# Optimization experiments

Hardware: AMD Instinct MI355X
Metric: run time of the kernel (lower is better)

The kernel has to match this reference:

```python
import jax, jax.numpy as jnp
import numpy as np

# Config: B sequences, each of length S; paged KV cache with NB blocks of size BS.
B, S, HQ, HK, D = 4, 1024, 32, 8, 128
BS = 256
NB = B * (S // BS)  # 16 blocks, one contiguous run per sequence
SCALE = 1.0 / float(np.sqrt(D))


def setup_inputs() -> dict:
    key = jax.random.key(0)
    k1, k2, k3 = jax.random.split(key, 3)
    q = jax.random.normal(k1, (B * S, HQ, D), dtype=jnp.float32)
    k_cache = jax.random.normal(k2, (NB, BS, HK, D), dtype=jnp.float32)
    v_cache = jax.random.normal(k3, (NB, BS, HK, D), dtype=jnp.float32)
    # block_table[b, j] = physical block id of j-th logical block of sequence b
    block_table = jnp.arange(B * (S // BS), dtype=jnp.int32).reshape(B, S // BS)
    return {"q": q, "k_cache": k_cache, "v_cache": v_cache, "block_table": block_table}


def reference(q, k_cache, v_cache, block_table):
    # Equivalent of pytorch_attn_varlen_func (prefill, causal, paged KV, GQA)
    # with equal per-sequence lengths, vectorized over the batch dim.
    Bn, nblk = block_table.shape
    _, BSc, Hk, Dd = k_cache.shape
    Sl = nblk * BSc
    Hq = q.shape[1]
    g = Hq // Hk  # GQA group size

    qb = q.reshape(Bn, Sl, Hq, Dd)  # [B, S, Hq, D]

    # Paged gather: token t -> block block_table[b, t // BS], offset t % BS
    t = jnp.arange(Sl)
    bids = block_table[:, t // BSc]          # [B, S]
    off = t % BSc                             # [S]
    kb = k_cache[bids, off[None, :]]          # [B, S, Hk, D]
    vb = v_cache[bids, off[None, :]]

    # Align KV heads to query heads (repeat_interleave over head dim)
    kb = jnp.repeat(kb, g, axis=2)            # [B, S, Hq, D]
    vb = jnp.repeat(vb, g, axis=2)

    scores = jnp.einsum('bqhd,bkhd->bhqk', qb, kb).astype(jnp.float32) * SCALE
    causal_mask = jnp.arange(Sl)[None, :] > jnp.arange(Sl)[:, None]  # [Sq, Sk]
    scores = jnp.where(causal_mask[None, None], -jnp.inf, scores)
    attn = jax.nn.softmax(scores, axis=-1).astype(q.dtype)  # [B, Hq, S, S]
    out = jnp.einsum('bhqk,bkhd->bqhd', attn, vb)            # [B, S, Hq, D]
    return out.reshape(Bn * Sl, Hq * Dd)
```

## Files before the change

kernel.cpp:

```cpp
#include <hip/hip_runtime.h>


#define SEQ   1024
#define NHQ   32
#define NHK   8
#define DH    128
#define BSZ   256
#define NBLK  16
#define QBLK  128
#define KVBLK 64
#define SCALE  0.0883883476483184f
#define SCLOG2 0.12752551286084812f

typedef __attribute__((ext_vector_type(8)))  short bf16x8;
typedef __attribute__((ext_vector_type(4)))  float f32x4;
typedef __attribute__((ext_vector_type(16))) float f32x16;
typedef __attribute__((ext_vector_type(2)))  unsigned int u32x2;
typedef unsigned short u16;
typedef unsigned int u32;
typedef unsigned long long u64;

static __device__ __forceinline__ u16 f2bf(float f) {
  union { float f; u32 u; } x; x.f = f;
  return (u16)((x.u + 0x7fffu + ((x.u >> 16) & 1u)) >> 16);
}

static __device__ __forceinline__ u32 cvtpk(float a, float b) {
  u32 r;
  asm("v_cvt_pk_bf16_f32 %0, %1, %2" : "=v"(r) : "v"(a), "v"(b));
  return r;
}

static __device__ __forceinline__ void gload16(const u16* src, u16* dst_lds) {
  __builtin_amdgcn_global_load_lds(
      (const __attribute__((address_space(1))) u32*)src,
      (__attribute__((address_space(3))) u32*)dst_lds, 16, 0, 0);
}

__global__ __launch_bounds__(256)
void prep_kv(const float* __restrict__ kc_, const float* __restrict__ vc_,
             u16* __restrict__ kb, u16* __restrict__ vbT) {
  __shared__ u16 lvt[64 * 132];

  const int t  = threadIdx.x;
  const int blk = blockIdx.x;
  const int t4 = blk & 3;
  const int hk = (blk >> 2) & 7;
  const int nb = blk >> 5;
  const int key0 = t4 * 64;

  const int d4 = t & 31;
  const int kr = t >> 5;

#pragma unroll
  for (int i = 0; i < 8; ++i) {
    const int key = kr + i * 8;
    const size_t srow = ((size_t)(nb * BSZ + key0 + key) * NHK + hk) * DH + 4 * d4;
    f32x4 kx = *(const f32x4*)(kc_ + srow);
    f32x4 vx = *(const f32x4*)(vc_ + srow);
    u64 pk = (u64)f2bf(kx[0]) | ((u64)f2bf(kx[1]) << 16) |
             ((u64)f2bf(kx[2]) << 32) | ((u64)f2bf(kx[3]) << 48);
    *(u64*)(kb + (((size_t)(nb * NHK + hk) * BSZ + key0 + key) * DH + 4 * d4)) = pk;
    u64 pv = (u64)f2bf(vx[0]) | ((u64)f2bf(vx[1]) << 16) |
             ((u64)f2bf(vx[2]) << 32) | ((u64)f2bf(vx[3]) << 48);
    *(u64*)&lvt[key * 132 + 4 * d4] = pv;
  }
  __syncthreads();

  const int d  = t >> 1;
  const int h2 = t & 1;
  u16* dst = vbT + ((size_t)(nb * NHK + hk) * DH + d) * BSZ + key0 + h2 * 32;
  u64 outw[8];
#pragma unroll
  for (int j = 0; j < 8; ++j) {
    const int kbase = h2 * 32 + j * 4;
    outw[j] = (u64)lvt[(kbase + 0) * 132 + d]
            | ((u64)lvt[(kbase + 1) * 132 + d] << 16)
            | ((u64)lvt[(kbase + 2) * 132 + d] << 32)
            | ((u64)lvt[(kbase + 3) * 132 + d] << 48);
  }
#pragma unroll
  for (int j = 0; j < 8; ++j) ((u64*)dst)[j] = outw[j];
}

__global__ __launch_bounds__(256, 2)
void attn_fwd_pre(const float* __restrict__ qg,
                  const u16* __restrict__ kbg,
                  const u16* __restrict__ vbT,
                  const int* __restrict__ btab,
                  float* __restrict__ outg)
{
  __shared__ u16 lk[2][KVBLK * DH];
  __shared__ u16 lv[2][DH * KVBLK];

  const int tid  = threadIdx.x;
  const int lane = tid & 63;
  const int w    = tid >> 6;
  const int ln   = lane & 31;
  const int hi   = lane >> 5;
  const int bid  = blockIdx.x;

  const int qc = 7 - (bid >> 7);
  const int rr = bid & 127;
  const int hq = rr >> 2;
  const int b  = rr & 3;
  const int hk = hq >> 2;

  const int rg = qc * QBLK + w * 32 + ln;

  bf16x8 qf[8];
  {
    const float* qp = qg + ((size_t)(b * SEQ + rg) * NHQ + hq) * DH;
#pragma unroll
    for (int dc = 0; dc < 8; ++dc) {
      const int d0 = dc * 16 + hi * 8;
      f32x4 x0 = *(const f32x4*)(qp + d0);
      f32x4 x1 = *(const f32x4*)(qp + d0 + 4);
      bf16x8 f;
#pragma unroll
      for (int j = 0; j < 4; ++j) {
        f[j]     = (short)f2bf(x0[j] * SCLOG2);
        f[j + 4] = (short)f2bf(x1[j] * SCLOG2);
      }
      qf[dc] = f;
    }
  }

  bf16x8 onesf;
#pragma unroll
  for (int j = 0; j < 8; ++j) onesf[j] = (short)0x3F80;

  f32x16 o[4];
#pragma unroll
  for (int db = 0; db < 4; ++db)
#pragma unroll
    for (int i = 0; i < 16; ++i) o[db][i] = 0.f;
  f32x16 lacc;
#pragma unroll
  for (int i = 0; i < 16; ++i) lacc[i] = 0.f;

  const u16* kbh = kbg + (size_t)hk * BSZ * DH;
  const u16* vbh = vbT + (size_t)hk * DH * BSZ;

  auto stage_k = [&](int t, int c) {
    const int nb   = btab[b * (SEQ / BSZ) + (t >> 2)];
    const int off0 = (t & 3) * KVBLK;
    const u16* ksrc = kbh + (size_t)nb * (NHK * BSZ * DH) + (size_t)off0 * DH;
#pragma unroll
    for (int i = 0; i < 4; ++i) {
      const int kbs = w * 16 + i * 4;
      const int key = kbs + (lane >> 4);
      const u16* src = ksrc + key * DH + 8 * ((lane & 15) ^ (key & 15));
      gload16(src, &lk[c][kbs * DH]);
    }
  };
  auto stage_v = [&](int t, int c) {
    const int nb   = btab[b * (SEQ / BSZ) + (t >> 2)];
    const int off0 = (t & 3) * KVBLK;
    const u16* vsrc = vbh + (size_t)nb * (NHK * DH * BSZ) + off0;
#pragma unroll
    for (int i = 0; i < 4; ++i) {
      const int dbs = w * 32 + i * 8;
      const int d   = dbs + (lane >> 3);
      const u16* src = vsrc + d * BSZ + 8 * ((lane & 7) ^ (d & 7));
      gload16(src, &lv[c][dbs * KVBLK]);
    }
  };

  const int ntile = 2 * qc + 2;
  const int tmaxw = 2 * qc + (w >> 1);

  auto qk = [&](int tt, int cc, f32x16& s0, f32x16& s1) {
    if (tt <= tmaxw) {
      __builtin_amdgcn_s_setprio(1);
#pragma unroll
      for (int kb = 0; kb < 2; ++kb) {
        f32x16 acc;
#pragma unroll
        for (int i = 0; i < 16; ++i) acc[i] = 0.f;
        const int key  = kb * 32 + ln;
        const int srow = key * DH;
        const int sw   = (key & 15) * 8;
#pragma unroll
        for (int dc = 0; dc < 8; ++dc) {
          const int d0 = dc * 16 + hi * 8;
          bf16x8 kf = *(const bf16x8*)&lk[cc][srow + (d0 ^ sw)];
          acc = __builtin_amdgcn_mfma_f32_32x32x16_bf16(kf, qf[dc], acc, 0, 0, 0);
        }
        if (kb == 0) s0 = acc; else s1 = acc;
      }
      __builtin_amdgcn_s_setprio(0);
      if (tt == tmaxw) {
        const int kt = tt * KVBLK;
#pragma unroll
        for (int r = 0; r < 16; ++r) {
          const int kg0 = kt + (r & 3) + 8 * (r >> 2) + 4 * hi;
          if (kg0 > rg)      s0[r] = -1e30f;
          if (kg0 + 32 > rg) s1[r] = -1e30f;
        }
      }
    } else {
#pragma unroll
      for (int i = 0; i < 16; ++i) { s0[i] = -1e30f; s1[i] = -1e30f; }
    }
  };

  auto pv = [&](f32x16& p0, f32x16& p1, int cc) {
#pragma unroll
    for (int kc = 0; kc < 4; ++kc) {
      const int cc2 = kc & 1;
      const f32x16& sa0 = (kc < 2) ? p0 : p1;
      const u32 x0 = cvtpk(sa0[8 * cc2 + 0], sa0[8 * cc2 + 1]);
      const u32 y0 = cvtpk(sa0[8 * cc2 + 4], sa0[8 * cc2 + 5]);
      const u32 x1 = cvtpk(sa0[8 * cc2 + 2], sa0[8 * cc2 + 3]);
      const u32 y1 = cvtpk(sa0[8 * cc2 + 6], sa0[8 * cc2 + 7]);
      u32x2 r0 = __builtin_amdgcn_permlane32_swap(x0, y0, false, false);
      u32x2 r1 = __builtin_amdgcn_permlane32_swap(x1, y1, false, false);
      union { bf16x8 v; u32 u[4]; } pb;
      pb.u[0] = r0[0]; pb.u[1] = r1[0]; pb.u[2] = r0[1]; pb.u[3] = r1[1];
      const int k0 = kc * 16 + hi * 8;
      __builtin_amdgcn_s_setprio(1);
#pragma unroll
      for (int db = 0; db < 4; ++db) {
        const int d = db * 32 + ln;
        bf16x8 vf = *(const bf16x8*)&lv[cc][d * KVBLK + (k0 ^ ((d & 7) * 8))];
        o[db] = __builtin_amdgcn_mfma_f32_32x32x16_bf16(vf, pb.v, o[db], 0, 0, 0);
      }
      lacc = __builtin_amdgcn_mfma_f32_32x32x16_bf16(onesf, pb.v, lacc, 0, 0, 0);
      __builtin_amdgcn_s_setprio(0);
    }
  };

  stage_k(0, 0);
  if (1 < ntile) stage_k(1, 1);
  stage_v(0, 0);
  if (1 < ntile) stage_v(1, 1);
  __syncthreads();

  for (int t = 0; t < ntile; t += 2) {
    const bool liveA = (t <= tmaxw);
    const bool liveB = (t + 1 <= tmaxw);

    f32x16 sA0, sA1, sB0, sB1;
    qk(t,     0, sA0, sA1);
    qk(t + 1, 1, sB0, sB1);

    __syncthreads();

    if (t + 2 < ntile) stage_k(t + 2, 0);
    if (t + 3 < ntile) stage_k(t + 3, 1);

    if (liveA) {
#pragma unroll
      for (int i = 0; i < 16; ++i) {
        sA0[i] = exp2f(sA0[i]);
        sA1[i] = exp2f(sA1[i]);
      }
      if (liveB) {
#pragma unroll
        for (int i = 0; i < 16; ++i) {
          sB0[i] = exp2f(sB0[i]);
          sB1[i] = exp2f(sB1[i]);
        }
      }

      pv(sA0, sA1, 0);
      if (liveB) pv(sB0, sB1, 1);
    }

    __syncthreads();

    if (t + 2 < ntile) stage_v(t + 2, 0);
    if (t + 3 < ntile) stage_v(t + 3, 1);
  }

  const float inv = 1.0f / lacc[0];
  float* op = outg + ((size_t)(b * SEQ + rg) * NHQ + hq) * DH;
#pragma unroll
  for (int db = 0; db < 4; ++db)
#pragma unroll
    for (int q4 = 0; q4 < 4; ++q4) {
      f32x4 val;
#pragma unroll
      for (int r2 = 0; r2 < 4; ++r2) val[r2] = o[db][q4 * 4 + r2] * inv;
      *(f32x4*)(op + db * 32 + q4 * 8 + hi * 4) = val;
    }
}

__global__ __launch_bounds__(256, 2)
void attn_fwd_fb(const float* __restrict__ qg,
                 const float* __restrict__ kcache,
                 const float* __restrict__ vcache,
                 const int*   __restrict__ btab,
                 float* __restrict__ outg)
{
  __shared__ u16 lk[KVBLK * DH];
  __shared__ u16 lv[DH * KVBLK];
  __shared__ u16 lp[4][16 * KVBLK];

  const int tid  = threadIdx.x;
  const int lane = tid & 63;
  const int w    = tid >> 6;
  const int qt   = blockIdx.x;
  const int hq   = blockIdx.y;
  const int b    = blockIdx.z;
  const int hk   = hq >> 2;
  const int qbase = qt * 64;
  const int cl = lane & 15;
  const int kg = lane >> 4;

  bf16x8 qf[4];
  {
    const int tq = qbase + w * 16 + cl;
    const float* qp = qg + ((size_t)(b * SEQ + tq) * NHQ + hq) * DH;
#pragma unroll
    for (int dc = 0; dc < 4; ++dc) {
      const int d0 = dc * 32 + kg * 8;
      f32x4 x0 = *(const f32x4*)(qp + d0);
      f32x4 x1 = *(const f32x4*)(qp + d0 + 4);
      bf16x8 f;
#pragma unroll
      for (int j = 0; j < 4; ++j) { f[j] = (short)f2bf(x0[j] * SCALE); f[j + 4] = (short)f2bf(x1[j] * SCALE); }
      qf[dc] = f;
    }
  }

  f32x4 o[8];
#pragma unroll
  for (int i = 0; i < 8; ++i) o[i] = (f32x4){0.f, 0.f, 0.f, 0.f};
  float mrow[4] = {-1e30f, -1e30f, -1e30f, -1e30f};
  float lrow[4] = {0.f, 0.f, 0.f, 0.f};

  const int ntile = qt + 1;
  for (int t = 0; t < ntile; ++t) {
    __syncthreads();
    {
      const int nb   = btab[b * (SEQ / BSZ) + ((t * KVBLK) / BSZ)];
      const int off0 = (t * KVBLK) % BSZ;
      const int d4 = tid & 31;
      const int kl = tid >> 5;
      const float* kbp = kcache + (((size_t)nb * BSZ + off0) * NHK + hk) * DH + d4 * 4;
      const float* vbp = vcache + (((size_t)nb * BSZ + off0) * NHK + hk) * DH + d4 * 4;
#pragma unroll
      for (int p = 0; p < 8; ++p) {
        const int key = p * 8 + kl;
        const size_t go = (size_t)key * (NHK * DH);
        f32x4 kx = *(const f32x4*)(kbp + go);
        f32x4 vx = *(const f32x4*)(vbp + go);
        u32 w0 = (u32)f2bf(kx[0]) | ((u32)f2bf(kx[1]) << 16);
        u32 w1 = (u32)f2bf(kx[2]) | ((u32)f2bf(kx[3]) << 16);
        const int doff = (4 * d4) ^ ((key & 7) * 8);
        u64 pk = (u64)w0 | ((u64)w1 << 32);
        *(u64*)&lk[key * DH + doff] = pk;
#pragma unroll
        for (int j = 0; j < 4; ++j) {
          const int d = 4 * d4 + j;
          lv[d * KVBLK + (key ^ ((d & 7) * 8))] = f2bf(vx[j]);
        }
      }
    }
    __syncthreads();

    float s[4][4];
#pragma unroll
    for (int ct = 0; ct < 4; ++ct) {
      f32x4 acc = (f32x4){0.f, 0.f, 0.f, 0.f};
      const int key = ct * 16 + cl;
#pragma unroll
      for (int dc = 0; dc < 4; ++dc) {
        const int d0 = (dc * 32 + kg * 8) ^ ((key & 7) * 8);
        bf16x8 kf = *(const bf16x8*)&lk[key * DH + d0];
        acc = __builtin_amdgcn_mfma_f32_16x16x32_bf16(qf[dc], kf, acc, 0, 0, 0);
      }
#pragma unroll
      for (int v = 0; v < 4; ++v) s[ct][v] = acc[v];
    }
    if (t == qt) {
      const int rbase = w * 16 + kg * 4;
#pragma unroll
      for (int ct = 0; ct < 4; ++ct) {
        const int key = ct * 16 + cl;
#pragma unroll
        for (int v = 0; v < 4; ++v)
          if (key > rbase + v) s[ct][v] = -1e30f;
      }
    }
    float corr[4];
#pragma unroll
    for (int v = 0; v < 4; ++v) {
      float x = fmaxf(fmaxf(s[0][v], s[1][v]), fmaxf(s[2][v], s[3][v]));
#pragma unroll
      for (int off = 1; off < 16; off <<= 1) x = fmaxf(x, __shfl_xor(x, off));
      const float mn = fmaxf(mrow[v], x);
      corr[v] = __expf(mrow[v] - mn);
      mrow[v] = mn;
    }
    float rs[4] = {0.f, 0.f, 0.f, 0.f};
    u16 pb[4][4];
#pragma unroll
    for (int ct = 0; ct < 4; ++ct)
#pragma unroll
      for (int v = 0; v < 4; ++v) {
        const float p = __expf(s[ct][v] - mrow[v]);
        rs[v] += p;
        pb[ct][v] = f2bf(p);
      }
#pragma unroll
    for (int v = 0; v < 4; ++v) {
      float x = rs[v];
#pragma unroll
      for (int off = 1; off < 16; off <<= 1) x += __shfl_xor(x, off);
      lrow[v] = lrow[v] * corr[v] + x;
    }
#pragma unroll
    for (int dt = 0; dt < 8; ++dt)
#pragma unroll
      for (int v = 0; v < 4; ++v) o[dt][v] *= corr[v];

    u16* pw = &lp[w][0];
#pragma unroll
    for (int ct = 0; ct < 4; ++ct)
#pragma unroll
      for (int v = 0; v < 4; ++v) {
        const int r = kg * 4 + v;
        const int cc = ct * 16 + cl;
        pw[r * KVBLK + (cc ^ ((r & 7) * 8))] = pb[ct][v];
      }
    bf16x8 pa[2];
#pragma unroll
    for (int kc2 = 0; kc2 < 2; ++kc2) {
      const int c0 = (kc2 * 32 + kg * 8) ^ ((cl & 7) * 8);
      pa[kc2] = *(const bf16x8*)&pw[cl * KVBLK + c0];
    }
#pragma unroll
    for (int dt = 0; dt < 8; ++dt) {
      const int d = dt * 16 + cl;
#pragma unroll
      for (int kc2 = 0; kc2 < 2; ++kc2) {
        const int c0 = (kc2 * 32 + kg * 8) ^ ((d & 7) * 8);
        bf16x8 vf = *(const bf16x8*)&lv[d * KVBLK + c0];
        o[dt] = __builtin_amdgcn_mfma_f32_16x16x32_bf16(pa[kc2], vf, o[dt], 0, 0, 0);
      }
    }
  }

#pragma unroll
  for (int v = 0; v < 4; ++v) {
    const float inv = 1.0f / lrow[v];
    const int tq = qbase + w * 16 + kg * 4 + v;
    float* op = outg + ((size_t)(b * SEQ + tq) * NHQ + hq) * DH;
#pragma unroll
    for (int dt = 0; dt < 8; ++dt) op[dt * 16 + cl] = o[dt][v] * inv;
  }
}

extern "C" void kernel_launch(void* const* d_in, const int* in_sizes, int n_in,
                              void* d_out, int out_size, void* d_ws, size_t ws_size,
                              hipStream_t stream) {
  const float* q  = (const float*)d_in[0];
  const float* kc = (const float*)d_in[1];
  const float* vc = (const float*)d_in[2];
  const int*   bt = (const int*)d_in[3];
  float* out = (float*)d_out;
  const size_t kv_elems = (size_t)NBLK * NHK * BSZ * DH;
  const size_t need = 2 * kv_elems * sizeof(u16);
  if (ws_size >= need) {
    u16* kb  = (u16*)d_ws;
    u16* vbT = kb + kv_elems;
    prep_kv<<<NBLK * NHK * 4, 256, 0, stream>>>(kc, vc, kb, vbT);
    attn_fwd_pre<<<dim3(1024), 256, 0, stream>>>(q, kb, vbT, bt, out);
  } else {
    dim3 grid_fb(SEQ / 64, NHQ, 4 );
    attn_fwd_fb<<<grid_fb, 256, 0, stream>>>(q, kc, vc, bt, out);
  }
}
```

Measured before the change: 78.01 us.

## Restructure KV loop to one tile per iteration with single-buffered V

Replaces the two-tiles-per-iteration loop, which double-buffered both K and V, with a one-tile loop. K stays double-buffered and is prefetched one tile ahead, while V is single-buffered and loaded at the start of each iteration so it overlaps the QK and exp work. This halves V's LDS footprint, which may help occupancy, and cuts register pressure from holding two score tiles. The cost is one barrier pair per tile instead of per two tiles, and V loads have less time to land before PV.

```diff
diff --git a/kernel.cpp b/kernel.cpp
--- a/kernel.cpp
+++ b/kernel.cpp
@@ -91,7 +91,7 @@
                   float* __restrict__ outg)
 {
   __shared__ u16 lk[2][KVBLK * DH];
-  __shared__ u16 lv[2][DH * KVBLK];
+  __shared__ u16 lv[DH * KVBLK];
 
   const int tid  = threadIdx.x;
   const int lane = tid & 63;
@@ -154,7 +154,7 @@
       gload16(src, &lk[c][kbs * DH]);
     }
   };
-  auto stage_v = [&](int t, int c) {
+  auto stage_v = [&](int t) {
     const int nb   = btab[b * (SEQ / BSZ) + (t >> 2)];
     const int off0 = (t & 3) * KVBLK;
     const u16* vsrc = vbh + (size_t)nb * (NHK * DH * BSZ) + off0;
@@ -163,15 +163,25 @@
       const int dbs = w * 32 + i * 8;
       const int d   = dbs + (lane >> 3);
       const u16* src = vsrc + d * BSZ + 8 * ((lane & 7) ^ (d & 7));
-      gload16(src, &lv[c][dbs * KVBLK]);
+      gload16(src, &lv[dbs * KVBLK]);
     }
   };
 
   const int ntile = 2 * qc + 2;
   const int tmaxw = 2 * qc + (w >> 1);
 
-  auto qk = [&](int tt, int cc, f32x16& s0, f32x16& s1) {
-    if (tt <= tmaxw) {
+  stage_k(0, 0);
+  __syncthreads();
+
+  for (int t = 0; t < ntile; ++t) {
+    const int c = t & 1;
+    const bool live = (t <= tmaxw);
+
+    stage_v(t);
+    if (t + 1 < ntile) stage_k(t + 1, c ^ 1);
+
+    f32x16 sa[2];
+    if (live) {
       __builtin_amdgcn_s_setprio(1);
 #pragma unroll
       for (int kb = 0; kb < 2; ++kb) {
@@ -184,94 +194,58 @@
 #pragma unroll
         for (int dc = 0; dc < 8; ++dc) {
           const int d0 = dc * 16 + hi * 8;
-          bf16x8 kf = *(const bf16x8*)&lk[cc][srow + (d0 ^ sw)];
+          bf16x8 kf = *(const bf16x8*)&lk[c][srow + (d0 ^ sw)];
           acc = __builtin_amdgcn_mfma_f32_32x32x16_bf16(kf, qf[dc], acc, 0, 0, 0);
         }
-        if (kb == 0) s0 = acc; else s1 = acc;
+        sa[kb] = acc;
       }
       __builtin_amdgcn_s_setprio(0);
-      if (tt == tmaxw) {
-        const int kt = tt * KVBLK;
+
+      if (t == tmaxw) {
+        const int kt = t * KVBLK;
 #pragma unroll
         for (int r = 0; r < 16; ++r) {
           const int kg0 = kt + (r & 3) + 8 * (r >> 2) + 4 * hi;
-          if (kg0 > rg)      s0[r] = -1e30f;
-          if (kg0 + 32 > rg) s1[r] = -1e30f;
+          if (kg0 > rg)      sa[0][r] = -1e30f;
+          if (kg0 + 32 > rg) sa[1][r] = -1e30f;
         }
       }
-    } else {
-#pragma unroll
-      for (int i = 0; i < 16; ++i) { s0[i] = -1e30f; s1[i] = -1e30f; }
-    }
-  };
-
-  auto pv = [&](f32x16& p0, f32x16& p1, int cc) {
-#pragma unroll
-    for (int kc = 0; kc < 4; ++kc) {
-      const int cc2 = kc & 1;
-      const f32x16& sa0 = (kc < 2) ? p0 : p1;
-      const u32 x0 = cvtpk(sa0[8 * cc2 + 0], sa0[8 * cc2 + 1]);
-      const u32 y0 = cvtpk(sa0[8 * cc2 + 4], sa0[8 * cc2 + 5]);
-      const u32 x1 = cvtpk(sa0[8 * cc2 + 2], sa0[8 * cc2 + 3]);
-      const u32 y1 = cvtpk(sa0[8 * cc2 + 6], sa0[8 * cc2 + 7]);
-      u32x2 r0 = __builtin_amdgcn_permlane32_swap(x0, y0, false, false);
-      u32x2 r1 = __builtin_amdgcn_permlane32_swap(x1, y1, false, false);
-      union { bf16x8 v; u32 u[4]; } pb;
-      pb.u[0] = r0[0]; pb.u[1] = r1[0]; pb.u[2] = r0[1]; pb.u[3] = r1[1];
-      const int k0 = kc * 16 + hi * 8;
-      __builtin_amdgcn_s_setprio(1);
-#pragma unroll
-      for (int db = 0; db < 4; ++db) {
-        const int d = db * 32 + ln;
-        bf16x8 vf = *(const bf16x8*)&lv[cc][d * KVBLK + (k0 ^ ((d & 7) * 8))];
-        o[db] = __builtin_amdgcn_mfma_f32_32x32x16_bf16(vf, pb.v, o[db], 0, 0, 0);
-      }
-      lacc = __builtin_amdgcn_mfma_f32_32x32x16_bf16(onesf, pb.v, lacc, 0, 0, 0);
-      __builtin_amdgcn_s_setprio(0);
-    }
-  };
-
-  stage_k(0, 0);
-  if (1 < ntile) stage_k(1, 1);
-  stage_v(0, 0);
-  if (1 < ntile) stage_v(1, 1);
-  __syncthreads();
-
-  for (int t = 0; t < ntile; t += 2) {
-    const bool liveA = (t <= tmaxw);
-    const bool liveB = (t + 1 <= tmaxw);
-
-    f32x16 sA0, sA1, sB0, sB1;
-    qk(t,     0, sA0, sA1);
-    qk(t + 1, 1, sB0, sB1);
+
+#pragma unroll
+      for (int i = 0; i < 16; ++i) {
+        sa[0][i] = exp2f(sa[0][i]);
+        sa[1][i] = exp2f(sa[1][i]);
+      }
+    }
 
     __syncthreads();
 
-    if (t + 2 < ntile) stage_k(t + 2, 0);
-    if (t + 3 < ntile) stage_k(t + 3, 1);
-
-    if (liveA) {
-#pragma unroll
-      for (int i = 0; i < 16; ++i) {
-        sA0[i] = exp2f(sA0[i]);
-        sA1[i] = exp2f(sA1[i]);
-      }
-      if (liveB) {
-#pragma unroll
-        for (int i = 0; i < 16; ++i) {
-          sB0[i] = exp2f(sB0[i]);
-          sB1[i] = exp2f(sB1[i]);
+    if (live) {
+#pragma unroll
+      for (int kc = 0; kc < 4; ++kc) {
+        const int kb = kc >> 1, cc2 = kc & 1;
+        const u32 x0 = cvtpk(sa[kb][8 * cc2 + 0], sa[kb][8 * cc2 + 1]);
+        const u32 y0 = cvtpk(sa[kb][8 * cc2 + 4], sa[kb][8 * cc2 + 5]);
+        const u32 x1 = cvtpk(sa[kb][8 * cc2 + 2], sa[kb][8 * cc2 + 3]);
+        const u32 y1 = cvtpk(sa[kb][8 * cc2 + 6], sa[kb][8 * cc2 + 7]);
+        u32x2 r0 = __builtin_amdgcn_permlane32_swap(x0, y0, false, false);
+        u32x2 r1 = __builtin_amdgcn_permlane32_swap(x1, y1, false, false);
+        union { bf16x8 v; u32 u[4]; } pb;
+        pb.u[0] = r0[0]; pb.u[1] = r1[0]; pb.u[2] = r0[1]; pb.u[3] = r1[1];
+        const int k0 = kc * 16 + hi * 8;
+        __builtin_amdgcn_s_setprio(1);
+#pragma unroll
+        for (int db = 0; db < 4; ++db) {
+          const int d = db * 32 + ln;
+          bf16x8 vf = *(const bf16x8*)&lv[d * KVBLK + (k0 ^ ((d & 7) * 8))];
+          o[db] = __builtin_amdgcn_mfma_f32_32x32x16_bf16(vf, pb.v, o[db], 0, 0, 0);
         }
-      }
-
-      pv(sA0, sA1, 0);
-      if (liveB) pv(sB0, sB1, 1);
+        lacc = __builtin_amdgcn_mfma_f32_32x32x16_bf16(onesf, pb.v, lacc, 0, 0, 0);
+        __builtin_amdgcn_s_setprio(0);
+      }
     }
 
     __syncthreads();
-
-    if (t + 2 < ntile) stage_v(t + 2, 0);
-    if (t + 3 < ntile) stage_v(t + 3, 1);
   }
 
   const float inv = 1.0f / lacc[0];
```

Measured after the change: 77.89 us. About the same (-0.2%).
